# Optimization experiments

Measured on AMD Instinct MI355X. Metric: run time of the kernel, lower is better.

Reference implementation:

```python
import jax, jax.numpy as jnp
import numpy as np


def _resize_axis_linear(x, new_size, axis):
    """1-D linear resize along `axis` with align_corners=True semantics."""
    old = x.shape[axis]
    if old == new_size:
        return x
    pos = jnp.arange(new_size, dtype=jnp.float32) * (float(old - 1) / float(max(new_size - 1, 1)))
    i0 = jnp.floor(pos).astype(jnp.int32)
    i1 = jnp.minimum(i0 + 1, old - 1)
    w = (pos - i0.astype(jnp.float32)).astype(x.dtype)
    shp = [1] * x.ndim
    shp[axis] = new_size
    w = w.reshape(shp)
    return jnp.take(x, i0, axis=axis) * (1 - w) + jnp.take(x, i1, axis=axis) * w


def bilinear_resize(x, out_h, out_w):
    # x: (B, h, w, C) -> (B, out_h, out_w, C), align_corners=True
    x = _resize_axis_linear(x, out_h, axis=1)
    x = _resize_axis_linear(x, out_w, axis=2)
    return x


def grid_sample_bilinear_border(feat, grid):
    """feat: (B,H,W,C); grid: (B,H',W',2) with (x,y) in [-1,1]; align_corners=True, border padding."""
    B, H, W, C = feat.shape
    ix = (grid[..., 0] + 1.0) * 0.5 * (W - 1)
    iy = (grid[..., 1] + 1.0) * 0.5 * (H - 1)
    ix = jnp.clip(ix, 0.0, W - 1)  # border padding
    iy = jnp.clip(iy, 0.0, H - 1)
    ix0 = jnp.floor(ix).astype(jnp.int32)
    iy0 = jnp.floor(iy).astype(jnp.int32)
    ix1 = jnp.minimum(ix0 + 1, W - 1)
    iy1 = jnp.minimum(iy0 + 1, H - 1)
    wx = (ix - ix0.astype(ix.dtype))[..., None]
    wy = (iy - iy0.astype(iy.dtype))[..., None]
    b = jnp.arange(B)[:, None, None]
    v00 = feat[b, iy0, ix0]
    v01 = feat[b, iy0, ix1]
    v10 = feat[b, iy1, ix0]
    v11 = feat[b, iy1, ix1]
    top = v00 * (1 - wx) + v01 * wx
    bot = v10 * (1 - wx) + v11 * wx
    return top * (1 - wy) + bot * wy


def _forward(features, H, W, W1, b1, W2, b2, weight_coef, pool_size=2):
    B, L, C = features.shape
    # ---- pool_patches: avg_pool2d(kernel=stride=pool_size) on (B,H,W,C) ----
    feat_map = features.reshape(B, H, W, C)
    Hp, Wp = H // pool_size, W // pool_size
    pooled = feat_map.reshape(B, Hp, pool_size, Wp, pool_size, C).mean(axis=(2, 4))  # (B,Hp,Wp,C)
    Lp = Hp * Wp
    pooled_flat = pooled.reshape(B, Lp, C)
    # ---- deform predictor MLP (GELU exact, matches torch default) ----
    h = jax.nn.gelu(pooled_flat @ W1 + b1, approximate=False)
    dp = (h @ W2 + b2) * weight_coef  # (B, Lp, 4)
    delta_x = jnp.tanh(dp[..., 0])
    delta_y = jnp.tanh(dp[..., 1])
    delta_w = jax.nn.softplus(dp[..., 2])
    delta_h = jax.nn.softplus(dp[..., 3])
    # ---- base normalized grid at pooled resolution ----
    gy, gx = jnp.meshgrid(jnp.arange(Hp, dtype=jnp.float32), jnp.arange(Wp, dtype=jnp.float32), indexing='ij')
    gx = 2.0 * gx / max(Wp - 1, 1) - 1.0
    gy = 2.0 * gy / max(Hp - 1, 1) - 1.0
    ox = gx.reshape(1, Lp)
    oy = gy.reshape(1, Lp)
    dx = jnp.clip(ox + delta_x * (2.0 / max(Wp, 1)), -1.0, 1.0)
    dy = jnp.clip(oy + delta_y * (2.0 / max(Hp, 1)), -1.0, 1.0)
    deformed_coords = jnp.stack([dx, dy], axis=-1)  # (B, Lp, 2)
    # ---- upsample coords to full res and grid-sample features ----
    coords_map = deformed_coords.reshape(B, Hp, Wp, 2)
    coords_full = bilinear_resize(coords_map, H, W)  # (B, H, W, 2)
    sampled = grid_sample_bilinear_border(feat_map, coords_full)  # (B, H, W, C)
    deformed_features = sampled.reshape(B, L, C)
    full_deform_params = jnp.stack([delta_x, delta_y, delta_w, delta_h], axis=-1)  # (B, Lp, 4)
    return deformed_features, full_deform_params, deformed_coords


def setup_inputs() -> dict:
    key = jax.random.key(0)
    ks = jax.random.split(key, 6)
    B, H, W, C = 16, 128, 128, 192
    hidden = max(C // 4, 64)
    features = jax.random.normal(ks[0], (B, H * W, C), dtype=jnp.float32)
    W1 = jax.random.normal(ks[1], (C, hidden), dtype=jnp.float32) * (1.0 / np.sqrt(C))
    b1 = jax.random.normal(ks[2], (hidden,), dtype=jnp.float32) * 0.01
    W2 = jax.random.normal(ks[3], (hidden, 4), dtype=jnp.float32) * (1.0 / np.sqrt(hidden))
    b2 = jax.random.normal(ks[4], (4,), dtype=jnp.float32) * 0.01
    weight_coef = jnp.ones((4,), dtype=jnp.float32)
    return {"features": features, "H": H, "W": W, "W1": W1, "b1": b1, "W2": W2, "b2": b2, "weight_coef": weight_coef}


def reference(features, H, W, W1, b1, W2, b2, weight_coef):
    return _forward(features, H, W, W1, b1, W2, b2, weight_coef)
```

## Files before the change

kernel.cpp:

```cpp
#include <hip/hip_runtime.h>
#include <math.h>

#define Bn   16
#define Hn   128
#define Wn   128
#define Cn   192
#define HPn  64
#define WPn  64
#define LPn  4096
#define Ln   16384
#define HIDn 64

__device__ __forceinline__ float gelu_exact(float x) {
    return 0.5f * x * (1.0f + erff(x * 0.70710678118654752440f));
}
__device__ __forceinline__ float softplus_f(float x) {
    return fmaxf(x, 0.0f) + log1pf(expf(-fabsf(x)));
}

__global__ __launch_bounds__(256)
void pool_mlp_kernel(const float* __restrict__ feat,
                     const float* __restrict__ W1,
                     const float* __restrict__ b1,
                     const float* __restrict__ W2,
                     const float* __restrict__ b2,
                     const float* __restrict__ wcoef,
                     float* __restrict__ out_params,
                     float* __restrict__ out_coords)
{
    __shared__ float s_pool[16][Cn];
    __shared__ float s_hid[16][HIDn];
    const int t = threadIdx.x;
    const int g0  = blockIdx.x * 16;
    const int b   = g0 >> 12;
    const int lp0 = g0 & 4095;
    const int hp  = lp0 >> 6;
    const int wp0 = lp0 & 63;

    const float* fb = feat + (size_t)b * Ln * Cn;
    const int h0 = hp * 2;

#pragma unroll
    for (int k = 0; k < 12; ++k) {
        int v = t + k * 256;
        int p = v / Cn;
        int c = v - p * Cn;
        int w0 = (wp0 + p) * 2;
        size_t base = ((size_t)h0 * Wn + w0) * Cn + c;
        float s = fb[base] + fb[base + Cn] + fb[base + (size_t)Wn * Cn] +
                  fb[base + (size_t)Wn * Cn + Cn];
        s_pool[p][c] = 0.25f * s;
    }
    __syncthreads();

    const int j  = t & 63;
    const int pb = t >> 6;
    float a0 = b1[j], a1 = a0, a2 = a0, a3 = a0;
    for (int c = 0; c < Cn; ++c) {
        float w = W1[c * HIDn + j];
        a0 = fmaf(s_pool[pb     ][c], w, a0);
        a1 = fmaf(s_pool[pb +  4][c], w, a1);
        a2 = fmaf(s_pool[pb +  8][c], w, a2);
        a3 = fmaf(s_pool[pb + 12][c], w, a3);
    }
    s_hid[pb     ][j] = gelu_exact(a0);
    s_hid[pb +  4][j] = gelu_exact(a1);
    s_hid[pb +  8][j] = gelu_exact(a2);
    s_hid[pb + 12][j] = gelu_exact(a3);
    __syncthreads();

    if (t < 64) {
        int p = t >> 2, k = t & 3;
        float acc = b2[k];
        for (int c = 0; c < HIDn; ++c)
            acc = fmaf(s_hid[p][c], W2[c * 4 + k], acc);
        float dp = acc * wcoef[k];
        float val = (k < 2) ? tanhf(dp) : softplus_f(dp);
        int lp = lp0 + p;
        out_params[((size_t)b * LPn + lp) * 4 + k] = val;
        if (k == 0) {
            float ox = 2.0f * (float)(wp0 + p) / 63.0f - 1.0f;
            float dx = ox + val * (2.0f / 64.0f);
            dx = fminf(fmaxf(dx, -1.0f), 1.0f);
            out_coords[((size_t)b * LPn + lp) * 2 + 0] = dx;
        } else if (k == 1) {
            float oy = 2.0f * (float)hp / 63.0f - 1.0f;
            float dy = oy + val * (2.0f / 64.0f);
            dy = fminf(fmaxf(dy, -1.0f), 1.0f);
            out_coords[((size_t)b * LPn + lp) * 2 + 1] = dy;
        }
    }
}

__global__ __launch_bounds__(256)
void sample_kernel(const float* __restrict__ feat,
                   const float* __restrict__ coords,
                   float* __restrict__ out)
{
    const int idx = blockIdx.x * 256 + threadIdx.x;
    const int pix = idx / 48;
    const int c4  = idx - pix * 48;
    const int b   = pix >> 14;
    const int rem = pix & 16383;
    const int i   = rem >> 7;
    const int jj  = rem & 127;

    const float sc = 63.0f / 127.0f;
    float py = i * sc, px = jj * sc;
    float fy0 = floorf(py), fx0 = floorf(px);
    float wy = py - fy0, wx = px - fx0;
    int iy0 = (int)fy0, ix0 = (int)fx0;
    int iy1 = min(iy0 + 1, 63), ix1 = min(ix0 + 1, 63);
    const float2* cm = (const float2*)coords + ((size_t)b << 12);
    float2 c00 = cm[iy0 * 64 + ix0];
    float2 c01 = cm[iy0 * 64 + ix1];
    float2 c10 = cm[iy1 * 64 + ix0];
    float2 c11 = cm[iy1 * 64 + ix1];
    float gx = (c00.x * (1.0f - wy) + c10.x * wy) * (1.0f - wx) +
               (c01.x * (1.0f - wy) + c11.x * wy) * wx;
    float gy = (c00.y * (1.0f - wy) + c10.y * wy) * (1.0f - wx) +
               (c01.y * (1.0f - wy) + c11.y * wy) * wx;

    float ix = (gx + 1.0f) * 0.5f * 127.0f;
    float iy = (gy + 1.0f) * 0.5f * 127.0f;
    ix = fminf(fmaxf(ix, 0.0f), 127.0f);
    iy = fminf(fmaxf(iy, 0.0f), 127.0f);
    float fx = floorf(ix), fy = floorf(iy);
    float swx = ix - fx, swy = iy - fy;
    int sx0 = (int)fx, sy0 = (int)fy;
    int sx1 = min(sx0 + 1, 127), sy1 = min(sy0 + 1, 127);

    const float4* f4 = (const float4*)feat + ((size_t)b << 14) * 48;
    float4 v00 = f4[(sy0 * 128 + sx0) * 48 + c4];
    float4 v01 = f4[(sy0 * 128 + sx1) * 48 + c4];
    float4 v10 = f4[(sy1 * 128 + sx0) * 48 + c4];
    float4 v11 = f4[(sy1 * 128 + sx1) * 48 + c4];

    float iwx = 1.0f - swx, iwy = 1.0f - swy;
    float4 r;
    r.x = (v00.x * iwx + v01.x * swx) * iwy + (v10.x * iwx + v11.x * swx) * swy;
    r.y = (v00.y * iwx + v01.y * swx) * iwy + (v10.y * iwx + v11.y * swx) * swy;
    r.z = (v00.z * iwx + v01.z * swx) * iwy + (v10.z * iwx + v11.z * swx) * swy;
    r.w = (v00.w * iwx + v01.w * swx) * iwy + (v10.w * iwx + v11.w * swx) * swy;
    ((float4*)out)[idx] = r;
}

extern "C" void kernel_launch(void* const* d_in, const int* in_sizes, int n_in,
                              void* d_out, int out_size, void* d_ws, size_t ws_size,
                              hipStream_t stream) {
    const float* feat = (const float*)d_in[0];
    const float* W1 = (const float*)d_in[3];
    const float* b1 = (const float*)d_in[4];
    const float* W2 = (const float*)d_in[5];
    const float* b2 = (const float*)d_in[6];
    const float* wc = (const float*)d_in[7];

    float* out        = (float*)d_out;
    float* out_params = out + (size_t)Bn * Ln * Cn;
    float* out_coords = out_params + (size_t)Bn * LPn * 4;

    pool_mlp_kernel<<<(Bn * LPn) / 16, 256, 0, stream>>>(
        feat, W1, b1, W2, b2, wc, out_params, out_coords);

    sample_kernel<<<(Bn * Hn * Wn * 48) / 256, 256, 0, stream>>>(
        feat, out_coords, out);
}
```

Before: 409.0 us.

## Vectorize pooling loads, remap sample blocks per XCD, and loop channels per thread

The pooling stage now reads float4 vectors and writes them to aligned shared memory instead of doing scalar loads. The sampling kernel maps each block to 16 pixels, with 16 threads per pixel each handling 3 float4 channel chunks. This computes the coordinate interpolation once per pixel rather than once per float4. Block indices are also swizzled so each batch image stays on one XCD, which aims to improve L2 locality of the gathered feature rows. The trade-off is fewer blocks and more work per thread, which could lower latency hiding.

```diff
diff --git a/kernel.cpp b/kernel.cpp
--- a/kernel.cpp
+++ b/kernel.cpp
@@ -28,7 +28,7 @@
                      float* __restrict__ out_params,
                      float* __restrict__ out_coords)
 {
-    __shared__ float s_pool[16][Cn];
+    __shared__ __align__(16) float s_pool[16][Cn];
     __shared__ float s_hid[16][HIDn];
     const int t = threadIdx.x;
     const int g0  = blockIdx.x * 16;
@@ -37,19 +37,24 @@
     const int hp  = lp0 >> 6;
     const int wp0 = lp0 & 63;
 
-    const float* fb = feat + (size_t)b * Ln * Cn;
+    const float4* fb4 = (const float4*)feat + ((size_t)b << 14) * 48;
     const int h0 = hp * 2;
 
 #pragma unroll
-    for (int k = 0; k < 12; ++k) {
-        int v = t + k * 256;
-        int p = v / Cn;
-        int c = v - p * Cn;
-        int w0 = (wp0 + p) * 2;
-        size_t base = ((size_t)h0 * Wn + w0) * Cn + c;
-        float s = fb[base] + fb[base + Cn] + fb[base + (size_t)Wn * Cn] +
-                  fb[base + (size_t)Wn * Cn + Cn];
-        s_pool[p][c] = 0.25f * s;
+    for (int it = 0; it < 3; ++it) {
+        int v  = t + it * 256;
+        int p  = v / 48;
+        int c4 = v - p * 48;
+        int x0 = (wp0 + p) * 2;
+        const float4* r0 = fb4 + ((size_t)h0 * Wn + x0) * 48 + c4;
+        const float4* r1 = r0 + (size_t)Wn * 48;
+        float4 a = r0[0], bb = r0[48], c = r1[0], d = r1[48];
+        float4 s;
+        s.x = 0.25f * (a.x + bb.x + c.x + d.x);
+        s.y = 0.25f * (a.y + bb.y + c.y + d.y);
+        s.z = 0.25f * (a.z + bb.z + c.z + d.z);
+        s.w = 0.25f * (a.w + bb.w + c.w + d.w);
+        *((float4*)&s_pool[p][c4 * 4]) = s;
     }
     __syncthreads();
 
@@ -97,13 +102,17 @@
                    const float* __restrict__ coords,
                    float* __restrict__ out)
 {
-    const int idx = blockIdx.x * 256 + threadIdx.x;
-    const int pix = idx / 48;
-    const int c4  = idx - pix * 48;
-    const int b   = pix >> 14;
-    const int rem = pix & 16383;
-    const int i   = rem >> 7;
-    const int jj  = rem & 127;
+    const int blk  = blockIdx.x;
+    const int xcd  = blk & 7;
+    const int slot = blk >> 3;
+    const int b    = xcd + ((slot >> 10) << 3);
+    const int tile = slot & 1023;
+    const int t = threadIdx.x;
+    const int p = t >> 4;
+    const int s = t & 15;
+    const int pix = tile * 16 + p;
+    const int i  = pix >> 7;
+    const int jj = pix & 127;
 
     const float sc = 63.0f / 127.0f;
     float py = i * sc, px = jj * sc;
@@ -129,20 +138,30 @@
     float swx = ix - fx, swy = iy - fy;
     int sx0 = (int)fx, sy0 = (int)fy;
     int sx1 = min(sx0 + 1, 127), sy1 = min(sy0 + 1, 127);
+    float iwx = 1.0f - swx, iwy = 1.0f - swy;
+    float w00 = iwx * iwy, w01 = swx * iwy, w10 = iwx * swy, w11 = swx * swy;
 
     const float4* f4 = (const float4*)feat + ((size_t)b << 14) * 48;
-    float4 v00 = f4[(sy0 * 128 + sx0) * 48 + c4];
-    float4 v01 = f4[(sy0 * 128 + sx1) * 48 + c4];
-    float4 v10 = f4[(sy1 * 128 + sx0) * 48 + c4];
-    float4 v11 = f4[(sy1 * 128 + sx1) * 48 + c4];
+    float4* o4 = (float4*)out + ((size_t)b << 14) * 48 + (size_t)pix * 48;
+    const int base00 = (sy0 * Wn + sx0) * 48;
+    const int base01 = (sy0 * Wn + sx1) * 48;
+    const int base10 = (sy1 * Wn + sx0) * 48;
+    const int base11 = (sy1 * Wn + sx1) * 48;
 
-    float iwx = 1.0f - swx, iwy = 1.0f - swy;
-    float4 r;
-    r.x = (v00.x * iwx + v01.x * swx) * iwy + (v10.x * iwx + v11.x * swx) * swy;
-    r.y = (v00.y * iwx + v01.y * swx) * iwy + (v10.y * iwx + v11.y * swx) * swy;
-    r.z = (v00.z * iwx + v01.z * swx) * iwy + (v10.z * iwx + v11.z * swx) * swy;
-    r.w = (v00.w * iwx + v01.w * swx) * iwy + (v10.w * iwx + v11.w * swx) * swy;
-    ((float4*)out)[idx] = r;
+#pragma unroll
+    for (int k = 0; k < 3; ++k) {
+        int c4 = s + k * 16;
+        float4 v00 = f4[base00 + c4];
+        float4 v01 = f4[base01 + c4];
+        float4 v10 = f4[base10 + c4];
+        float4 v11 = f4[base11 + c4];
+        float4 r;
+        r.x = v00.x * w00 + v01.x * w01 + v10.x * w10 + v11.x * w11;
+        r.y = v00.y * w00 + v01.y * w01 + v10.y * w10 + v11.y * w11;
+        r.z = v00.z * w00 + v01.z * w01 + v10.z * w10 + v11.z * w11;
+        r.w = v00.w * w00 + v01.w * w01 + v10.w * w10 + v11.w * w11;
+        o4[c4] = r;
+    }
 }
 
 extern "C" void kernel_launch(void* const* d_in, const int* in_sizes, int n_in,
@@ -162,6 +181,5 @@
     pool_mlp_kernel<<<(Bn * LPn) / 16, 256, 0, stream>>>(
         feat, W1, b1, W2, b2, wc, out_params, out_coords);
 
-    sample_kernel<<<(Bn * Hn * Wn * 48) / 256, 256, 0, stream>>>(
-        feat, out_coords, out);
+    sample_kernel<<<Bn * 1024, 256, 0, stream>>>(feat, out_coords, out);
 }
```

Result: no change. 411.2 us (+0.5%).
